# Performance work log

Hardware: AMD Instinct MI355X
Metric: run time of the kernel (lower is better)

## Reference

```python
import jax, jax.numpy as jnp
import numpy as np

GROUP_SIZE = 128  # per-group quantization granularity along K


def setup_inputs() -> dict:
    key = jax.random.key(0)
    k1, k2, k3, k4 = jax.random.split(key, 4)
    B, S, K, N = 4, 2048, 4096, 11008
    num_groups = K // GROUP_SIZE
    x = jax.random.normal(k1, (B, S, K), dtype=jnp.float16)
    # packed uint4 pairs stored as bytes (values 0..255); int32 stands in for uint8
    weight = jax.random.randint(k2, (N, K // 2), 0, 256, dtype=jnp.int32)
    scale = jax.random.uniform(k3, (N, num_groups), dtype=jnp.float16, minval=0.001, maxval=0.02)
    bias = jax.random.normal(k4, (N,), dtype=jnp.float16)
    return {"x": x, "weight": weight, "scale": scale, "bias": bias}


def _dequant_int4(weight, scale):
    # weight: [N, K//2] packed bytes; low nibble = even k, high nibble = odd k
    N, Kh = weight.shape
    K = Kh * 2
    low = (weight & 15) - 8          # [N, K//2], signed int4 in [-8, 7]
    high = ((weight >> 4) & 15) - 8  # [N, K//2]
    w_int4 = jnp.stack([low, high], axis=-1).reshape(N, K).astype(jnp.float32)
    # broadcast per-group scales along K: [N, num_groups] -> [N, K]
    s = jnp.repeat(scale.astype(jnp.float32), GROUP_SIZE, axis=1)
    return w_int4 * s  # [N, K] fp32


def reference(x, weight, scale, bias):
    # out = x @ dequant(w).T + bias, fp32 accumulation, fp16 store (as in kernel)
    w_fp = _dequant_int4(weight, scale)                     # [N, K]
    acc = jnp.einsum('bsk,nk->bsn', x.astype(jnp.float32), w_fp)
    acc = acc + bias.astype(jnp.float32)[None, None, :]
    return acc.astype(jnp.float16)
```

## Files before the change

kernel.cpp:

```cpp
#include <hip/hip_runtime.h>

#define DEVINL __device__ __forceinline__

typedef __bf16 bf16x8 __attribute__((ext_vector_type(8)));
typedef float  f32x4  __attribute__((ext_vector_type(4)));

constexpr int KK = 4096;
constexpr int NN = 11008;
constexpr int NG = 32;

DEVINL unsigned short f2bf(float f){
  union { float f; unsigned u; } v; v.f = f;
  unsigned r = v.u + 0x7FFF + ((v.u >> 16) & 1);
  return (unsigned short)(r >> 16);
}
DEVINL unsigned pack2(float lo, float hi){
  return (unsigned)f2bf(lo) | ((unsigned)f2bf(hi) << 16);
}
DEVINL void gload16(const void* g, void* l){
  __builtin_amdgcn_global_load_lds(
      (const __attribute__((address_space(1))) void*)g,
      (__attribute__((address_space(3))) void*)l, 16, 0, 0);
}

__global__ __launch_bounds__(256) void k_dequant(const int* __restrict__ W,
                                                 const float* __restrict__ S,
                                                 unsigned short* __restrict__ WB){
  int t = blockIdx.x * 256 + threadIdx.x;
  int row = t >> 9;
  int kp0 = (t & 511) << 2;
  int g   = kp0 >> 6;
  float s = S[row * NG + g];
  const int4 p = reinterpret_cast<const int4*>(W)[t];
  const int* pb = reinterpret_cast<const int*>(&p);
  unsigned q[4];
  #pragma unroll
  for (int i = 0; i < 4; ++i){
    int b = pb[i];
    float lo = ((float)(b & 15)        - 8.0f) * s;
    float hi = ((float)((b >> 4) & 15) - 8.0f) * s;
    q[i] = pack2(lo, hi);
  }
  reinterpret_cast<int4*>(WB)[t] = make_int4((int)q[0], (int)q[1], (int)q[2], (int)q[3]);
}

__global__ __launch_bounds__(256) void k_cvtA(const float* __restrict__ X,
                                              unsigned short* __restrict__ XB){
  int t = blockIdx.x * 256 + threadIdx.x;
  const float4* src = reinterpret_cast<const float4*>(X) + (size_t)t * 2;
  float4 a = src[0], b = src[1];
  reinterpret_cast<int4*>(XB)[t] = make_int4(
      (int)pack2(a.x, a.y), (int)pack2(a.z, a.w),
      (int)pack2(b.x, b.y), (int)pack2(b.z, b.w));
}

constexpr int BM2 = 256, BN2 = 256, BK2 = 64;
constexpr int HBY = 16384;
constexpr int BUFBY = 65536;

#define WAIT0  asm volatile("s_waitcnt vmcnt(0)" ::: "memory")
#define BAR()  do { __builtin_amdgcn_s_barrier(); asm volatile("" ::: "memory"); } while (0)

__global__ __launch_bounds__(512, 1) void k_gemm8c(const unsigned short* __restrict__ A,
                                                   const unsigned short* __restrict__ B,
                                                   const float* __restrict__ Bias,
                                                   float* __restrict__ C){
  __shared__ char smem[131072];
  const int tid = threadIdx.x, lane = tid & 63, wid = tid >> 6;
  const int wm = wid >> 2, wn = wid & 3;
  const int lr = lane & 15, hi = lane >> 4;
  const int cpx = gridDim.x >> 3;
  const int wg  = (blockIdx.x & 7) * cpx + (blockIdx.x >> 3);
  const int NTT = NN / BN2;
  const int mt = wg / NTT, nt = wg % NTT;
  const char* Ab = (const char*)(A + (size_t)mt * BM2 * KK);
  const char* Bb = (const char*)(B + (size_t)nt * BN2 * KK);
  const int srow  = tid >> 3;
  const int scolb = (tid & 7) * 16;

  auto stage_half = [&](int buf, int sel, int kt){
    const char* base = ((sel >= 2) ? Bb : Ab) + (size_t)((sel & 1) * 128) * KK * 2;
    #pragma unroll
    for (int r = 0; r < 2; ++r){
      int row = r * 64 + srow;
      const char* src = base + (size_t)row * (KK * 2) + kt * (BK2 * 2)
                      + (scolb ^ ((row & 7) << 4));
      char* dst = smem + buf * BUFBY + sel * HBY + r * 8192 + tid * 16;
      gload16(src, dst);
    }
  };
  auto frag = [&](int buf, int sel, int row, int bcol) -> bf16x8 {
    return *reinterpret_cast<const bf16x8*>(
        smem + buf * BUFBY + sel * HBY + row * 128 + (bcol ^ ((row & 7) << 4)));
  };

  const int selA = wm;
  const int selB = 2 + (wn >> 1);
  const int cB0  = (wn & 1) * 64;

  f32x4 acc[8][4] = {};

  stage_half(0, 0, 0); stage_half(0, 1, 0);
  stage_half(0, 2, 0); stage_half(0, 3, 0);
  WAIT0;
  BAR();

  const int NT = KK / BK2;
  for (int t = 0; t < NT; ++t){
    const int buf = t & 1;
    const bool pf = (t + 1 < NT);
    if (pf){
      stage_half(buf ^ 1, 0, t + 1);
      stage_half(buf ^ 1, 1, t + 1);
      stage_half(buf ^ 1, 2, t + 1);
      stage_half(buf ^ 1, 3, t + 1);
    }
    #pragma unroll
    for (int ks = 0; ks < 2; ++ks){
      bf16x8 af[8], bf[4];
      #pragma unroll
      for (int i = 0; i < 8; ++i)
        af[i] = frag(buf, selA, i*16 + lr, ks*64 + hi*16);
      #pragma unroll
      for (int j = 0; j < 4; ++j)
        bf[j] = frag(buf, selB, cB0 + j*16 + lr, ks*64 + hi*16);
      __builtin_amdgcn_s_setprio(1);
      #pragma unroll
      for (int i = 0; i < 8; ++i)
        #pragma unroll
        for (int j = 0; j < 4; ++j)
          acc[i][j] = __builtin_amdgcn_mfma_f32_16x16x32_bf16(af[i], bf[j], acc[i][j], 0, 0, 0);
      __builtin_amdgcn_s_setprio(0);
    }
    if (pf) WAIT0;
    BAR();
  }

  const int cmb = mt * BM2, cnb = nt * BN2;
  #pragma unroll
  for (int j = 0; j < 4; ++j){
    int col = cnb + wn * 64 + j * 16 + lr;
    float bv = Bias[col];
    #pragma unroll
    for (int i = 0; i < 8; ++i){
      int row0 = cmb + wm * 128 + i * 16 + hi * 4;
      #pragma unroll
      for (int r = 0; r < 4; ++r)
        C[(size_t)(row0 + r) * NN + col] = acc[i][j][r] + bv;
    }
  }
}

constexpr int BM = 128, BN = 128, BK = 32;
__global__ __launch_bounds__(256) void k_gemm_ws(const float* __restrict__ A,
                                                 const unsigned short* __restrict__ B,
                                                 const float* __restrict__ Bias,
                                                 float* __restrict__ C){
  __shared__ unsigned short As[2][BM][BK];
  __shared__ unsigned short Bs[2][BN][BK];
  const int tid = threadIdx.x;
  const int NT = NN / BN;
  const int mt = blockIdx.x / NT, nt = blockIdx.x % NT;
  const float*          Ab = A + (size_t)mt * BM * KK;
  const unsigned short* Bb = B + (size_t)nt * BN * KK;
  const int lane = tid & 63, wid = tid >> 6;
  const int wm = wid >> 1, wn = wid & 1;
  const int lr = lane & 15, lk = (lane >> 4) << 3;

  auto ld = [&](int kt, float4* ra, int4* rb){
    #pragma unroll
    for (int r = 0; r < 2; ++r){
      int c = r * 256 + tid, row = c >> 2, k0 = (c & 3) << 3;
      const float* src = Ab + (size_t)row * KK + kt * BK + k0;
      ra[2*r]   = *reinterpret_cast<const float4*>(src);
      ra[2*r+1] = *reinterpret_cast<const float4*>(src + 4);
      rb[r] = *reinterpret_cast<const int4*>(Bb + (size_t)row * KK + kt * BK + k0);
    }
  };
  auto st = [&](int buf, const float4* ra, const int4* rb){
    #pragma unroll
    for (int r = 0; r < 2; ++r){
      int c = r * 256 + tid, row = c >> 2, k0 = (c & 3) << 3;
      unsigned q[4];
      #pragma unroll
      for (int i = 0; i < 4; ++i)
        q[i] = pack2(ra[2*r + (i >> 1)][(i & 1) * 2], ra[2*r + (i >> 1)][(i & 1) * 2 + 1]);
      *reinterpret_cast<int4*>(&As[buf][row][k0]) =
          make_int4((int)q[0], (int)q[1], (int)q[2], (int)q[3]);
      *reinterpret_cast<int4*>(&Bs[buf][row][k0]) = rb[r];
    }
  };

  f32x4 acc[4][4] = {};
  {
    float4 ra[4]; int4 rb[2];
    ld(0, ra, rb);
    st(0, ra, rb);
  }
  __syncthreads();
  const int KT = KK / BK;
  for (int kt = 0; kt < KT; ++kt){
    int cur = kt & 1;
    float4 na[4]; int4 nb[2];
    if (kt + 1 < KT) ld(kt + 1, na, nb);
    bf16x8 af[4], bfr[4];
    #pragma unroll
    for (int i = 0; i < 4; ++i)
      af[i] = *reinterpret_cast<const bf16x8*>(&As[cur][wm*64 + i*16 + lr][lk]);
    #pragma unroll
    for (int i = 0; i < 4; ++i)
      bfr[i] = *reinterpret_cast<const bf16x8*>(&Bs[cur][wn*64 + i*16 + lr][lk]);
    #pragma unroll
    for (int i = 0; i < 4; ++i)
      #pragma unroll
      for (int j = 0; j < 4; ++j)
        acc[i][j] = __builtin_amdgcn_mfma_f32_16x16x32_bf16(af[i], bfr[j], acc[i][j], 0, 0, 0);
    if (kt + 1 < KT) st(cur ^ 1, na, nb);
    __syncthreads();
  }
  const int cm = mt * BM + wm * 64;
  const int cn = nt * BN + wn * 64;
  float bv[4];
  #pragma unroll
  for (int j = 0; j < 4; ++j) bv[j] = Bias[cn + j*16 + lr];
  #pragma unroll
  for (int i = 0; i < 4; ++i)
    #pragma unroll
    for (int j = 0; j < 4; ++j)
      #pragma unroll
      for (int r = 0; r < 4; ++r){
        size_t rr = (size_t)(cm + i*16 + (lane >> 4)*4 + r);
        C[rr * NN + (cn + j*16 + lr)] = acc[i][j][r] + bv[j];
      }
}

extern "C" void kernel_launch(void* const* d_in, const int* in_sizes, int n_in,
                              void* d_out, int out_size, void* d_ws, size_t ws_size,
                              hipStream_t stream){
  const float* x    = (const float*)d_in[0];
  const int*   w    = (const int*)d_in[1];
  const float* s    = (const float*)d_in[2];
  const float* bias = (const float*)d_in[3];
  float* out = (float*)d_out;
  const int M = in_sizes[0] / KK;
  const size_t needW = (size_t)NN * KK * 2;
  const size_t needA = (size_t)M * KK * 2;
  const int dq_blocks = (NN * (KK / 8)) / 256;

  if (ws_size >= needW + needA && (M % BM2) == 0){
    unsigned short* wb = (unsigned short*)d_ws;
    unsigned short* xb = (unsigned short*)((char*)d_ws + needW);
    k_dequant<<<dq_blocks, 256, 0, stream>>>(w, s, wb);
    k_cvtA<<<(M * (KK / 8)) / 256, 256, 0, stream>>>(x, xb);
    const int grid8 = (M / BM2) * (NN / BN2);
    k_gemm8c<<<grid8, 512, 0, stream>>>(xb, wb, bias, out);
  } else {
    unsigned short* wb = (unsigned short*)d_ws;
    k_dequant<<<dq_blocks, 256, 0, stream>>>(w, s, wb);
    const int grid = (M / BM) * (NN / BN);
    k_gemm_ws<<<grid, 256, 0, stream>>>(x, wb, bias, out);
  }
}
```

Measured before the change: 768.6 us.

## Ping-pong pipeline GEMM: split tile into quadrants with staggered loads and partial waits

```diff
diff --git a/kernel.cpp b/kernel.cpp
--- a/kernel.cpp
+++ b/kernel.cpp
@@ -58,16 +58,16 @@
 constexpr int HBY = 16384;
 constexpr int BUFBY = 65536;
 
-#define WAIT0  asm volatile("s_waitcnt vmcnt(0)" ::: "memory")
+#define VW(N)  asm volatile("s_waitcnt vmcnt(" #N ")" ::: "memory")
 #define BAR()  do { __builtin_amdgcn_s_barrier(); asm volatile("" ::: "memory"); } while (0)
 
-__global__ __launch_bounds__(512, 1) void k_gemm8c(const unsigned short* __restrict__ A,
-                                                   const unsigned short* __restrict__ B,
-                                                   const float* __restrict__ Bias,
-                                                   float* __restrict__ C){
+__global__ __launch_bounds__(512, 1) void k_gemm_pl(const unsigned short* __restrict__ A,
+                                                    const unsigned short* __restrict__ B,
+                                                    const float* __restrict__ Bias,
+                                                    float* __restrict__ C){
   __shared__ char smem[131072];
   const int tid = threadIdx.x, lane = tid & 63, wid = tid >> 6;
-  const int wm = wid >> 2, wn = wid & 3;
+  const int wr = wid >> 2, wc = wid & 3;
   const int lr = lane & 15, hi = lane >> 4;
   const int cpx = gridDim.x >> 3;
   const int wg  = (blockIdx.x & 7) * cpx + (blockIdx.x >> 3);
@@ -94,56 +94,91 @@
         smem + buf * BUFBY + sel * HBY + row * 128 + (bcol ^ ((row & 7) << 4)));
   };
 
-  const int selA = wm;
-  const int selB = 2 + (wn >> 1);
-  const int cB0  = (wn & 1) * 64;
-
+  bf16x8 A0a[4][2], B0a[2][2], A0b[4][2], B0b[2][2];
+  bf16x8 A1f[4][2], B1f[2][2];
   f32x4 acc[8][4] = {};
 
-  stage_half(0, 0, 0); stage_half(0, 1, 0);
-  stage_half(0, 2, 0); stage_half(0, 3, 0);
-  WAIT0;
+  auto rdA = [&](int buf, int sel, bf16x8 (&d)[4][2]){
+    #pragma unroll
+    for (int i = 0; i < 4; ++i)
+      #pragma unroll
+      for (int ks = 0; ks < 2; ++ks)
+        d[i][ks] = frag(buf, sel, wr*64 + i*16 + lr, ks*64 + hi*16);
+  };
+  auto rdB = [&](int buf, int sel, bf16x8 (&d)[2][2]){
+    #pragma unroll
+    for (int j = 0; j < 2; ++j)
+      #pragma unroll
+      for (int ks = 0; ks < 2; ++ks)
+        d[j][ks] = frag(buf, sel, wc*32 + j*16 + lr, ks*64 + hi*16);
+  };
+  auto MM = [&](const bf16x8 (&X)[4][2], const bf16x8 (&Y)[2][2], int qm, int qn){
+    __builtin_amdgcn_s_setprio(1);
+    #pragma unroll
+    for (int i = 0; i < 4; ++i)
+      #pragma unroll
+      for (int j = 0; j < 2; ++j)
+        #pragma unroll
+        for (int ks = 0; ks < 2; ++ks)
+          acc[qm*4 + i][qn*2 + j] = __builtin_amdgcn_mfma_f32_16x16x32_bf16(
+              X[i][ks], Y[j][ks], acc[qm*4 + i][qn*2 + j], 0, 0, 0);
+    __builtin_amdgcn_s_setprio(0);
+  };
+
+  stage_half(0, 2, 0); stage_half(0, 0, 0);
+  stage_half(0, 3, 0); stage_half(0, 1, 0);
+  VW(0);
   BAR();
+  rdA(0, 0, A0a); rdB(0, 2, B0a);
 
   const int NT = KK / BK2;
-  for (int t = 0; t < NT; ++t){
-    const int buf = t & 1;
-    const bool pf = (t + 1 < NT);
-    if (pf){
-      stage_half(buf ^ 1, 0, t + 1);
-      stage_half(buf ^ 1, 1, t + 1);
-      stage_half(buf ^ 1, 2, t + 1);
-      stage_half(buf ^ 1, 3, t + 1);
-    }
-    #pragma unroll
-    for (int ks = 0; ks < 2; ++ks){
-      bf16x8 af[8], bf[4];
-      #pragma unroll
-      for (int i = 0; i < 8; ++i)
-        af[i] = frag(buf, selA, i*16 + lr, ks*64 + hi*16);
-      #pragma unroll
-      for (int j = 0; j < 4; ++j)
-        bf[j] = frag(buf, selB, cB0 + j*16 + lr, ks*64 + hi*16);
-      __builtin_amdgcn_s_setprio(1);
-      #pragma unroll
-      for (int i = 0; i < 8; ++i)
-        #pragma unroll
-        for (int j = 0; j < 4; ++j)
-          acc[i][j] = __builtin_amdgcn_mfma_f32_16x16x32_bf16(af[i], bf[j], acc[i][j], 0, 0, 0);
-      __builtin_amdgcn_s_setprio(0);
-    }
-    if (pf) WAIT0;
-    BAR();
-  }
+
+  #define TILE(BUF, CA, CB, NA, NB, T)                                         \
+    do {                                                                       \
+      const bool pf = ((T) + 1 < NT);                                          \
+                                 \
+      rdB((BUF), 3, B1f);                                                      \
+      if (pf){ stage_half((BUF)^1, 2, (T)+1); stage_half((BUF)^1, 0, (T)+1); } \
+      if (pf) VW(4); else VW(0);                                               \
+      BAR();                                                                   \
+      MM((CA), (CB), 0, 0);                                                    \
+      BAR();                                                                   \
+                                                 \
+      rdA((BUF), 1, A1f);                                                      \
+      VW(2);                                                                   \
+      BAR();                                                                   \
+      MM((CA), B1f, 0, 1);                                                     \
+      BAR();                                                                   \
+                                \
+      if (pf) rdB((BUF)^1, 2, (NB));                                           \
+      if (pf) stage_half((BUF)^1, 3, (T)+1);                                   \
+      VW(2);                                                                   \
+      BAR();                                                                   \
+      MM(A1f, B1f, 1, 1);                                                      \
+      BAR();                                                                   \
+                                \
+      if (pf) rdA((BUF)^1, 0, (NA));                                           \
+      if (pf) stage_half((BUF)^1, 1, (T)+1);                                   \
+      VW(2);                                                                   \
+      BAR();                                                                   \
+      MM(A1f, (CB), 1, 0);                                                     \
+      BAR();                                                                   \
+    } while (0)
+
+  for (int t = 0; t < NT; t += 2){
+    TILE(0, A0a, B0a, A0b, B0b, t);
+    TILE(1, A0b, B0b, A0a, B0a, t + 1);
+  }
+  #undef TILE
 
   const int cmb = mt * BM2, cnb = nt * BN2;
   #pragma unroll
   for (int j = 0; j < 4; ++j){
-    int col = cnb + wn * 64 + j * 16 + lr;
+    int col = cnb + (j >> 1) * 128 + wc * 32 + (j & 1) * 16 + lr;
     float bv = Bias[col];
     #pragma unroll
     for (int i = 0; i < 8; ++i){
-      int row0 = cmb + wm * 128 + i * 16 + hi * 4;
+      int row0 = cmb + (i >> 2) * 128 + wr * 64 + (i & 3) * 16 + hi * 4;
       #pragma unroll
       for (int r = 0; r < 4; ++r)
         C[(size_t)(row0 + r) * NN + col] = acc[i][j][r] + bv;
@@ -253,7 +288,7 @@
     k_dequant<<<dq_blocks, 256, 0, stream>>>(w, s, wb);
     k_cvtA<<<(M * (KK / 8)) / 256, 256, 0, stream>>>(x, xb);
     const int grid8 = (M / BM2) * (NN / BN2);
-    k_gemm8c<<<grid8, 512, 0, stream>>>(xb, wb, bias, out);
+    k_gemm_pl<<<grid8, 512, 0, stream>>>(xb, wb, bias, out);
   } else {
     unsigned short* wb = (unsigned short*)d_ws;
     k_dequant<<<dq_blocks, 256, 0, stream>>>(w, s, wb);
```

After: 2.930 ms. 281% more time.
